# Optimization experiments

Hardware: AMD Instinct MI355X
Metric: run time of the kernel (lower is better)

Reference implementation:

```python
import jax, jax.numpy as jnp
import numpy as np

B, N, D, H, E, S, K, O = 32, 4096, 64, 64, 65536, 2, 2, 128
F = D + H                      # input_size = input_dim + hid_dim
M = S * K + 1                  # num_matrices


def setup_inputs() -> dict:
    key = jax.random.key(0)
    ks = jax.random.split(key, 7)
    inputs = jax.random.normal(ks[0], (B, N * D), dtype=jnp.float32)
    state = jax.random.normal(ks[1], (B, N * H), dtype=jnp.float32)
    # two sparse random-walk supports in COO form (rows, cols, vals)
    sup_rows = jax.random.randint(ks[2], (S, E), 0, N, dtype=jnp.int32)
    sup_cols = jax.random.randint(ks[3], (S, E), 0, N, dtype=jnp.int32)
    sup_vals = jax.random.uniform(ks[4], (S, E), dtype=jnp.float32) / 16.0
    # xavier_normal_ with gain=1.414
    std = 1.414 * np.sqrt(2.0 / (F * M + O))
    weight = jax.random.normal(ks[5], (F * M, O), dtype=jnp.float32) * std
    biases = jnp.zeros((O,), dtype=jnp.float32)  # bias_start = 0.0
    return {"inputs": inputs, "state": state, "sup_rows": sup_rows,
            "sup_cols": sup_cols, "sup_vals": sup_vals,
            "weight": weight, "biases": biases, "output_size": O}


def reference(inputs, state, sup_rows, sup_cols, sup_vals, weight, biases, output_size):
    b = inputs.shape[0]
    x_in = inputs.reshape(b, N, -1)
    st = state.reshape(b, N, -1)
    x = jnp.concatenate([x_in, st], axis=2)          # [B, N, F]
    f = x.shape[2]
    # [B,N,F] -> [N,F,B] -> [N, F*B]
    x0 = jnp.transpose(x, (1, 2, 0)).reshape(N, f * b)

    def spmm(s, m):
        # y[r] += v * m[c]  (sparse support @ dense)
        return jax.ops.segment_sum(sup_vals[s][:, None] * m[sup_cols[s]],
                                   sup_rows[s], num_segments=N)

    xs = [x0]
    for s in range(sup_vals.shape[0]):
        x1 = spmm(s, x0)
        xs.append(x1)
        xk_1, xk_2 = x1, x0
        for _ in range(2, K + 1):
            x2 = 2.0 * spmm(s, xk_1) - xk_2   # Chebyshev recurrence
            xs.append(x2)
            xk_1, xk_2 = x2, xk_1

    m = len(xs)
    # [M,N,F*B] -> [M,N,F,B] -> [B,N,F,M] -> [B*N, F*M]
    xc = jnp.stack(xs).reshape(m, N, f, b)
    xc = jnp.transpose(xc, (3, 1, 2, 0)).reshape(b * N, f * m)
    out = xc @ weight + biases                       # [B*N, O]
    return out.reshape(b, N * output_size)
```

## Files before the change

### kernel.cpp

```cpp
#include <hip/hip_runtime.h>
#include <hip/hip_bf16.h>

#define Bv 32
#define Nv 4096
#define Dv 64
#define Hv 64
#define Fv 128
#define Ev 65536
#define Sv 2
#define Ov 128
#define Mv 5

typedef unsigned int uint;
using short8  = __attribute__((ext_vector_type(8))) short;
using floatx4 = __attribute__((ext_vector_type(4))) float;
using f32x2   = __attribute__((ext_vector_type(2))) float;
using uintx4  = __attribute__((ext_vector_type(4))) uint;

#define AS1 __attribute__((address_space(1)))
#define AS3 __attribute__((address_space(3)))

__device__ __forceinline__ float bflo(uint u){ uint v = u << 16; float f; __builtin_memcpy(&f, &v, 4); return f; }
__device__ __forceinline__ float bfhi(uint u){ uint v = u & 0xffff0000u; float f; __builtin_memcpy(&f, &v, 4); return f; }
__device__ __forceinline__ unsigned short f2bf(float f){
  uint x; __builtin_memcpy(&x, &f, 4);
  x += 0x7fffu + ((x >> 16) & 1u);
  return (unsigned short)(x >> 16);
}
__device__ __forceinline__ uint bfpack(float a, float b){
  return (uint)f2bf(a) | ((uint)f2bf(b) << 16);
}

__device__ __forceinline__ void ld16(void* lds, const void* g){
  __builtin_amdgcn_global_load_lds((const AS1 uint*)g, (AS3 uint*)lds, 16, 0, 0);
}

__global__ void k_zero(int* __restrict__ p, int n){
  int i = blockIdx.x * 256 + threadIdx.x;
  if(i < n) p[i] = 0;
}

__global__ void k_hist(const int* __restrict__ rows, int* __restrict__ deg){
  int i = blockIdx.x * 256 + threadIdx.x;
  int s = i >> 16;
  int r = rows[i];
  atomicAdd(&deg[s * Nv + r], 1);
}

__global__ void k_scan(const int* __restrict__ deg, int* __restrict__ rowptr, int* __restrict__ cursor){
  __shared__ int part[256];
  __shared__ int sbase[256];
  int t = threadIdx.x;
  for(int s = 0; s < Sv; s++){
    int loc[16]; int sum = 0;
    #pragma unroll
    for(int i = 0; i < 16; i++){ loc[i] = deg[s * Nv + t * 16 + i]; sum += loc[i]; }
    part[t] = sum;
    __syncthreads();
    if(t == 0){ int run = 0; for(int i = 0; i < 256; i++){ int v = part[i]; sbase[i] = run; run += v; } }
    __syncthreads();
    int run = sbase[t];
    #pragma unroll
    for(int i = 0; i < 16; i++){
      int idx = t * 16 + i;
      rowptr[s * (Nv + 1) + idx] = run;
      cursor[s * Nv + idx] = run;
      run += loc[i];
    }
    if(t == 255) rowptr[s * (Nv + 1) + Nv] = run;
    __syncthreads();
  }
}

__global__ void k_scatter(const int* __restrict__ rows, const int* __restrict__ cols,
                          const float* __restrict__ vals, int* __restrict__ cursor,
                          uint* __restrict__ pk){
  int i = blockIdx.x * 256 + threadIdx.x;
  int s = i >> 16;
  int r = rows[i];
  int p = atomicAdd(&cursor[s * Nv + r], 1);
  pk[(s << 16) + p] = (uint)cols[i] | ((uint)f2bf(vals[i]) << 16);
}

__global__ void k_buildx0(const float* __restrict__ inp, const float* __restrict__ st,
                          uint* __restrict__ X0bf, uint* __restrict__ X08){
  const int t = blockIdx.x * 256 + threadIdx.x;
  const int c = t & 7;
  const int n = (t >> 3) & (Nv - 1);
  const int b = t >> 15;
  const float* src = (c < 4) ? (inp + ((size_t)b * Nv + n) * 64 + c * 16)
                             : (st  + ((size_t)b * Nv + n) * 64 + (c - 4) * 16);
  float v[16];
  #pragma unroll
  for(int q = 0; q < 4; q++){
    float4 f4 = *(const float4*)(src + q * 4);
    v[q * 4 + 0] = f4.x; v[q * 4 + 1] = f4.y; v[q * 4 + 2] = f4.z; v[q * 4 + 3] = f4.w;
  }
  const size_t base = (size_t)b * Nv + n;
  uint bfw[8];
  #pragma unroll
  for(int q = 0; q < 8; q++) bfw[q] = bfpack(v[2 * q], v[2 * q + 1]);
  *(uintx4*)(X0bf + base * 64 + c * 8)     = *(uintx4*)(bfw);
  *(uintx4*)(X0bf + base * 64 + c * 8 + 4) = *(uintx4*)(bfw + 4);
  uint f8w[4];
  #pragma unroll
  for(int q = 0; q < 4; q++){
    int w = __builtin_amdgcn_cvt_pk_fp8_f32(v[4 * q + 0], v[4 * q + 1], 0, false);
    w     = __builtin_amdgcn_cvt_pk_fp8_f32(v[4 * q + 2], v[4 * q + 3], w, true);
    f8w[q] = (uint)w;
  }
  *(uintx4*)(X08 + base * 32 + c * 4) = *(uintx4*)(f8w);
}

__global__ void k_wb(const float* __restrict__ wg, unsigned short* __restrict__ Wb){
  int t = blockIdx.x * 256 + threadIdx.x;
  if(t >= Mv * Ov * Fv) return;
  int f = t & (Fv - 1);
  int o = (t >> 7) & (Ov - 1);
  int m = t >> 14;
  Wb[t] = f2bf(wg[(f * Mv + m) * Ov + o]);
}

__launch_bounds__(256)
__global__ void k_spmm3(const uint* __restrict__ src8,
                        uint* __restrict__ dstA, uint* __restrict__ dstB,
                        uint* __restrict__ dA8, uint* __restrict__ dB8,
                        const uint* __restrict__ xprev,
                        const int* __restrict__ rowptr, const uint* __restrict__ pk,
                        const int two_supports){
  const int lane = threadIdx.x & 63;
  const int wv   = threadIdx.x >> 6;
  int bid = blockIdx.x;
  int s = 0;
  if(two_supports){ s = bid >> 12; bid &= 4095; }
  const int pg = bid & 3;
  const int r  = (bid >> 2) * 4 + wv;
  const int p  = pg * 8 + (lane >> 3);
  const int cB = (lane & 7) * 16;
  const int* rp   = rowptr + s * (Nv + 1);
  const uint* pks = pk + (s << 16);
  const int j0 = rp[r], j1 = rp[r + 1];
  const uint* gb = src8 + (size_t)p * Nv * 32 + (cB >> 2);
  uint* dst = s ? dstB : dstA;
  uint* d8  = s ? dB8  : dA8;

  float acc[16];
  #pragma unroll
  for(int k = 0; k < 16; k++) acc[k] = 0.f;

  for(int j = j0; j < j1; j += 64){
    int rem = j1 - j; if(rem > 64) rem = 64;
    const uint e = (lane < rem) ? pks[j + lane] : 0u;
    for(int t = 0; t < rem; t += 8){
      uintx4 g[8]; float v[8];
      #pragma unroll
      for(int u = 0; u < 8; u++){
        const uint eu = __shfl(e, t + u, 64);
        v[u] = bfhi(eu);
        const uint col = eu & 0xffffu;
        g[u] = *(const uintx4*)(gb + (size_t)col * 32);
      }
      #pragma unroll
      for(int u = 0; u < 8; u++){
        #pragma unroll
        for(int d = 0; d < 4; d++){
          f32x2 lo = __builtin_amdgcn_cvt_pk_f32_fp8((int)g[u][d], false);
          f32x2 hi = __builtin_amdgcn_cvt_pk_f32_fp8((int)g[u][d], true);
          acc[d * 4 + 0] += v[u] * lo[0];
          acc[d * 4 + 1] += v[u] * lo[1];
          acc[d * 4 + 2] += v[u] * hi[0];
          acc[d * 4 + 3] += v[u] * hi[1];
        }
      }
    }
  }

  const size_t obase = (size_t)p * Nv + r;
  if(xprev){
    const uint* pv = xprev + obase * 64 + (cB >> 1);
    uint pw[8];
    *(uintx4*)(pw)     = *(const uintx4*)(pv);
    *(uintx4*)(pw + 4) = *(const uintx4*)(pv + 4);
    #pragma unroll
    for(int q = 0; q < 8; q++){
      acc[2 * q + 0] = 2.f * acc[2 * q + 0] - bflo(pw[q]);
      acc[2 * q + 1] = 2.f * acc[2 * q + 1] - bfhi(pw[q]);
    }
  }
  uint bfw[8];
  #pragma unroll
  for(int q = 0; q < 8; q++) bfw[q] = bfpack(acc[2 * q], acc[2 * q + 1]);
  uint* db = dst + obase * 64 + (cB >> 1);
  __builtin_nontemporal_store(*(uintx4*)(bfw),     (uintx4*)(db));
  __builtin_nontemporal_store(*(uintx4*)(bfw + 4), (uintx4*)(db + 4));
  if(d8){
    uint f8w[4];
    #pragma unroll
    for(int q = 0; q < 4; q++){
      int w = __builtin_amdgcn_cvt_pk_fp8_f32(acc[4 * q + 0], acc[4 * q + 1], 0, false);
      w     = __builtin_amdgcn_cvt_pk_fp8_f32(acc[4 * q + 2], acc[4 * q + 3], w, true);
      f8w[q] = (uint)w;
    }
    __builtin_nontemporal_store(*(uintx4*)(f8w), (uintx4*)(d8 + obase * 32 + (cB >> 2)));
  }
}

__launch_bounds__(256)
__global__ void k_gemm(const unsigned short* __restrict__ X0,
                       const unsigned short* __restrict__ X1a,
                       const unsigned short* __restrict__ X2a,
                       const unsigned short* __restrict__ X1b,
                       const unsigned short* __restrict__ X2b,
                       const unsigned short* __restrict__ Wb,
                       const float* __restrict__ bias,
                       float* __restrict__ out){
  __shared__ unsigned short Asm[128 * 32];
  __shared__ unsigned short Bsm[128 * 32];
  const unsigned short* Am[5] = {X0, X1a, X2a, X1b, X2b};
  const int tid  = threadIdx.x;
  const int lane = tid & 63, wv = tid >> 6;
  const int wm = wv >> 1, wn = wv & 1;
  const int lrow = lane & 15, quad = lane >> 4;
  const size_t r0 = (size_t)blockIdx.x * 128;

  floatx4 acc[4][4] = {};

  #pragma unroll
  for(int m = 0; m < 5; m++){
    const unsigned short* Ab = Am[m] + r0 * Fv;
    const unsigned short* Bb = Wb + m * (Ov * Fv);
    #pragma unroll
    for(int kk = 0; kk < Fv; kk += 32){
      __syncthreads();
      #pragma unroll
      for(int p = 0; p < 2; p++){
        const int base_idx = p * 256 + wv * 64;
        const int my_idx = base_idx + lane;
        const int row = my_idx >> 2, seg = my_idx & 3;
        ld16(&Asm[base_idx * 8], Ab + (size_t)row * Fv + kk + seg * 8);
        ld16(&Bsm[base_idx * 8], Bb + row * Fv + kk + seg * 8);
      }
      __syncthreads();
      short8 af[4], bfr[4];
      #pragma unroll
      for(int t = 0; t < 4; t++){
        af[t]  = *(const short8*)(&Asm[(wm * 64 + t * 16 + lrow) * 32 + quad * 8]);
        bfr[t] = *(const short8*)(&Bsm[(wn * 64 + t * 16 + lrow) * 32 + quad * 8]);
      }
      #pragma unroll
      for(int ti = 0; ti < 4; ti++)
        #pragma unroll
        for(int tj = 0; tj < 4; tj++)
          acc[ti][tj] = __builtin_amdgcn_mfma_f32_16x16x32_bf16(af[ti], bfr[tj], acc[ti][tj], 0, 0, 0);
    }
  }

  #pragma unroll
  for(int ti = 0; ti < 4; ti++){
    #pragma unroll
    for(int tj = 0; tj < 4; tj++){
      const int col = wn * 64 + tj * 16 + lrow;
      const float bv = bias[col];
      const size_t rbase = r0 + wm * 64 + ti * 16 + quad * 4;
      #pragma unroll
      for(int t = 0; t < 4; t++){
        out[(rbase + t) * Ov + col] = acc[ti][tj][t] + bv;
      }
    }
  }
}

extern "C" void kernel_launch(void* const* d_in, const int* in_sizes, int n_in,
                              void* d_out, int out_size, void* d_ws, size_t ws_size,
                              hipStream_t stream) {
  (void)in_sizes; (void)n_in; (void)out_size; (void)ws_size;
  const float* inp  = (const float*)d_in[0];
  const float* st   = (const float*)d_in[1];
  const int*   rows = (const int*)d_in[2];
  const int*   cols = (const int*)d_in[3];
  const float* vals = (const float*)d_in[4];
  const float* wght = (const float*)d_in[5];
  const float* bias = (const float*)d_in[6];
  float* out = (float*)d_out;

  char* w = (char*)d_ws;
  const size_t SZX  = (size_t)Bv * Nv * Fv * 2;
  const size_t SZX8 = (size_t)Bv * Nv * Fv;
  unsigned short* X0  = (unsigned short*)(w);
  unsigned short* X1a = (unsigned short*)(w + SZX);
  unsigned short* X2a = (unsigned short*)(w + 2 * SZX);
  unsigned short* X1b = (unsigned short*)(w + 3 * SZX);
  unsigned short* X2b = (unsigned short*)(w + 4 * SZX);
  uint* X08  = (uint*)(w + 5 * SZX);
  uint* X1a8 = (uint*)(w + 5 * SZX + SZX8);
  uint* X1b8 = (uint*)(w + 5 * SZX + 2 * SZX8);
  unsigned short* Wb = (unsigned short*)(w + 5 * SZX + 3 * SZX8);
  char* p2 = w + 5 * SZX + 3 * SZX8 + 262144;
  int* deg    = (int*)p2;
  int* cursor = deg + Sv * Nv;
  int* rowptr = cursor + Sv * Nv;
  uint* pk    = (uint*)(rowptr + Sv * (Nv + 1) + 62);

  k_zero<<<(Sv * Nv + 255) / 256, 256, 0, stream>>>(deg, Sv * Nv);
  k_hist<<<Sv * Ev / 256, 256, 0, stream>>>(rows, deg);
  k_scan<<<1, 256, 0, stream>>>(deg, rowptr, cursor);
  k_scatter<<<Sv * Ev / 256, 256, 0, stream>>>(rows, cols, vals, cursor, pk);
  k_buildx0<<<(Bv * Nv * 8) / 256, 256, 0, stream>>>(inp, st, (uint*)X0, X08);
  k_wb<<<(Mv * Ov * Fv + 255) / 256, 256, 0, stream>>>(wght, Wb);

  k_spmm3<<<8192, 256, 0, stream>>>(X08, (uint*)X1a, (uint*)X1b, X1a8, X1b8,
                                    (const uint*)nullptr, rowptr, pk, 1);
  k_spmm3<<<4096, 256, 0, stream>>>(X1a8, (uint*)X2a, (uint*)X2a, nullptr, nullptr,
                                    (const uint*)X0, rowptr, pk, 0);
  k_spmm3<<<4096, 256, 0, stream>>>(X1b8, (uint*)X2b, (uint*)X2b, nullptr, nullptr,
                                    (const uint*)X0, rowptr + (Nv + 1), pk + Ev, 0);

  k_gemm<<<(Bv * Nv) / 128, 256, 0, stream>>>(X0, X1a, X2a, X1b, X2b, Wb, bias, out);
}
```

Baseline: 338.2 us.

## Double-buffer LDS tiles in GEMM to overlap loads with MFMA

The GEMM main loop now alternates between two LDS buffers, issuing the next stage's global-to-LDS loads before computing on the current buffer. This removes one of the two barriers per k-step and lets memory latency hide behind MFMA work. It also raises wave priority around the MFMA block, adds an occupancy hint to launch bounds, and writes outputs with nontemporal stores. LDS use per block doubles, which may reduce occupancy, and correctness depends on whether ld16 completes before the single barrier.

```diff
diff --git a/kernel.cpp b/kernel.cpp
--- a/kernel.cpp
+++ b/kernel.cpp
@@ -205,7 +205,7 @@
   }
 }
 
-__launch_bounds__(256)
+__launch_bounds__(256, 4)
 __global__ void k_gemm(const unsigned short* __restrict__ X0,
                        const unsigned short* __restrict__ X1a,
                        const unsigned short* __restrict__ X2a,
@@ -214,8 +214,8 @@
                        const unsigned short* __restrict__ Wb,
                        const float* __restrict__ bias,
                        float* __restrict__ out){
-  __shared__ unsigned short Asm[128 * 32];
-  __shared__ unsigned short Bsm[128 * 32];
+  __shared__ unsigned short Asm[2][128 * 32];
+  __shared__ unsigned short Bsm[2][128 * 32];
   const unsigned short* Am[5] = {X0, X1a, X2a, X1b, X2b};
   const int tid  = threadIdx.x;
   const int lane = tid & 63, wv = tid >> 6;
@@ -223,37 +223,47 @@
   const int lrow = lane & 15, quad = lane >> 4;
   const size_t r0 = (size_t)blockIdx.x * 128;
 
+  const int row0 = (wv * 64 + lane) >> 2, seg0 = (wv * 64 + lane) & 3;
+  const int row1 = (256 + wv * 64 + lane) >> 2, seg1 = (256 + wv * 64 + lane) & 3;
+  const int ldsb0 = (wv * 64) * 8;
+  const int ldsb1 = (256 + wv * 64) * 8;
+
   floatx4 acc[4][4] = {};
 
-  #pragma unroll
-  for(int m = 0; m < 5; m++){
-    const unsigned short* Ab = Am[m] + r0 * Fv;
-    const unsigned short* Bb = Wb + m * (Ov * Fv);
-    #pragma unroll
-    for(int kk = 0; kk < Fv; kk += 32){
-      __syncthreads();
+  #define STAGE(stp, bufi)                                                        \
+    do {                                                                          \
+      const int m_ = (stp) >> 2, kk_ = ((stp) & 3) * 32;                          \
+      const unsigned short* Ab_ = Am[m_] + r0 * Fv;                               \
+      const unsigned short* Bb_ = Wb + m_ * (Ov * Fv);                            \
+      ld16(&Asm[bufi][ldsb0], Ab_ + (size_t)row0 * Fv + kk_ + seg0 * 8);          \
+      ld16(&Bsm[bufi][ldsb0], Bb_ + row0 * Fv + kk_ + seg0 * 8);                  \
+      ld16(&Asm[bufi][ldsb1], Ab_ + (size_t)row1 * Fv + kk_ + seg1 * 8);          \
+      ld16(&Bsm[bufi][ldsb1], Bb_ + row1 * Fv + kk_ + seg1 * 8);                  \
+    } while (0)
+
+  STAGE(0, 0);
+  __syncthreads();
+
+  #pragma unroll
+  for(int step = 0; step < 20; ++step){
+    const int buf = step & 1;
+    if(step + 1 < 20) STAGE(step + 1, buf ^ 1);
+    short8 af[4], bfr[4];
+    #pragma unroll
+    for(int t = 0; t < 4; t++){
+      af[t]  = *(const short8*)(&Asm[buf][(wm * 64 + t * 16 + lrow) * 32 + quad * 8]);
+      bfr[t] = *(const short8*)(&Bsm[buf][(wn * 64 + t * 16 + lrow) * 32 + quad * 8]);
+    }
+    __builtin_amdgcn_s_setprio(1);
+    #pragma unroll
+    for(int ti = 0; ti < 4; ti++)
       #pragma unroll
-      for(int p = 0; p < 2; p++){
-        const int base_idx = p * 256 + wv * 64;
-        const int my_idx = base_idx + lane;
-        const int row = my_idx >> 2, seg = my_idx & 3;
-        ld16(&Asm[base_idx * 8], Ab + (size_t)row * Fv + kk + seg * 8);
-        ld16(&Bsm[base_idx * 8], Bb + row * Fv + kk + seg * 8);
-      }
-      __syncthreads();
-      short8 af[4], bfr[4];
-      #pragma unroll
-      for(int t = 0; t < 4; t++){
-        af[t]  = *(const short8*)(&Asm[(wm * 64 + t * 16 + lrow) * 32 + quad * 8]);
-        bfr[t] = *(const short8*)(&Bsm[(wn * 64 + t * 16 + lrow) * 32 + quad * 8]);
-      }
-      #pragma unroll
-      for(int ti = 0; ti < 4; ti++)
-        #pragma unroll
-        for(int tj = 0; tj < 4; tj++)
-          acc[ti][tj] = __builtin_amdgcn_mfma_f32_16x16x32_bf16(af[ti], bfr[tj], acc[ti][tj], 0, 0, 0);
-    }
-  }
+      for(int tj = 0; tj < 4; tj++)
+        acc[ti][tj] = __builtin_amdgcn_mfma_f32_16x16x32_bf16(af[ti], bfr[tj], acc[ti][tj], 0, 0, 0);
+    __builtin_amdgcn_s_setprio(0);
+    if(step + 1 < 20) __syncthreads();
+  }
+  #undef STAGE
 
   #pragma unroll
   for(int ti = 0; ti < 4; ti++){
@@ -264,7 +274,7 @@
       const size_t rbase = r0 + wm * 64 + ti * 16 + quad * 4;
       #pragma unroll
       for(int t = 0; t < 4; t++){
-        out[(rbase + t) * Ov + col] = acc[ti][tj][t] + bv;
+        __builtin_nontemporal_store(acc[ti][tj][t] + bv, &out[(rbase + t) * Ov + col]);
       }
     }
   }
```

New measurement: 331.5 us. 2.0% less time.
